# Optimization experiments

Measured on AMD Instinct MI355X. Metric: run time of the kernel, lower is better.

The kernel has to match this reference:

```python
import jax, jax.numpy as jnp
import numpy as np

B, C_IN, H, W = 8, 64, 256, 256
C_OUT, K, GROUPS, REP_DIM = 64, 3, 64, 512


def setup_inputs() -> dict:
    key = jax.random.key(0)
    k1, k2, k3 = jax.random.split(key, 3)
    x = jax.random.normal(k1, (B, C_IN, H, W), dtype=jnp.float32)
    representation = jax.random.normal(k2, (B, REP_DIM), dtype=jnp.float32)
    # Linear(representation_dim -> out_channels*k*k, bias=False) weight, [out_features, in_features]
    w_key = jax.random.normal(k3, (C_OUT * K * K, REP_DIM), dtype=jnp.float32) * (REP_DIM ** -0.5)
    return {"x": x, "representation": representation, "w_key": w_key}


def reference(x, representation, w_key):
    b = x.shape[0]
    fpg = C_IN // GROUPS          # features_per_group (input channels per group)
    opg = C_OUT // GROUPS         # output channels per group
    pad = K // 2

    # compress_key: Linear (no bias) + LeakyReLU(0.1)
    # per-sample dynamic kernels: [b, out_channels, k, k] (the repeat_interleave in the
    # original just copies this single spatial kernel across all fpg in-channels of a group)
    kern = jax.nn.leaky_relu(representation @ w_key.T, negative_slope=0.1)
    kern = kern.reshape(b, GROUPS, opg, K, K)

    # reflection pad (matches torch ReflectionPad2d)
    xp = jnp.pad(x, ((0, 0), (0, 0), (pad, pad), (pad, pad)), mode='reflect')

    # since each output channel's kernel is identical across its group's in-channels,
    # conv(sum of group channels) == sum of convs: pre-sum in-channels per group
    xg = xp.reshape(b, GROUPS, fpg, H + 2 * pad, W + 2 * pad).sum(axis=2)  # [b,g,hp,wp]

    # accumulate over the K*K kernel taps (small fixed loop), fully vectorized over b,g,h,w
    out = jnp.zeros((b, GROUPS, opg, H, W), dtype=x.dtype)
    for dy in range(K):
        for dx in range(K):
            out = out + jnp.einsum('bghw,bgo->bgohw',
                                   xg[:, :, dy:dy + H, dx:dx + W],
                                   kern[:, :, :, dy, dx])
    return out.reshape(b, C_OUT, H, W)
```

## Files before the change

kernel.cpp:

```cpp
#include <hip/hip_runtime.h>

typedef float f32x4 __attribute__((ext_vector_type(4)));

#define B_  8
#define C_  64
#define H_  256
#define W_  256
#define REP_ 512


#define RING 8
#define RPW  32

__global__ __launch_bounds__(256) void dwconv3x3_stream(const float* __restrict__ x,
                                                        const float* __restrict__ rep,
                                                        const float* __restrict__ wkey,
                                                        float* __restrict__ out) {
    int plane = blockIdx.x >> 1;
    int half  = blockIdx.x & 1;
    int wv   = threadIdx.x >> 6;
    int lane = threadIdx.x & 63;
    int b = plane >> 6;
    int c = plane & 63;

    __shared__ float kk[9];
    const float* rrow = rep + (size_t)b * REP_;
    for (int i = wv; i < 9; i += 4) {
        const float* wrow = wkey + (size_t)(c * 9 + i) * REP_;
        float acc = 0.f;
#pragma unroll
        for (int t = 0; t < REP_ / 64; ++t)
            acc += rrow[lane + t * 64] * wrow[lane + t * 64];
#pragma unroll
        for (int off = 32; off > 0; off >>= 1)
            acc += __shfl_xor(acc, off, 64);
        if (lane == 0)
            kk[i] = acc > 0.f ? acc : 0.1f * acc;
    }
    __syncthreads();

    float k[9];
#pragma unroll
    for (int i = 0; i < 9; ++i) k[i] = kk[i];

    int r0 = half * 128 + wv * RPW;
    int c4 = lane << 2;

    const float* pin  = x   + (size_t)plane * (H_ * W_);
    float*       pout = out + (size_t)plane * (H_ * W_);

    f32x4 raw[RING];
    float lft[RING], rgt[RING];

    auto issue = [&](int i) {
        int t = r0 - 1 + i;
        int rr = (t < 0) ? -t : ((t >= H_) ? (2 * H_ - 2 - t) : t);
        raw[i & 7] = *(const f32x4*)(pin + (size_t)rr * W_ + c4);
    };
    auto prep = [&](int i) {
        int s = i & 7;
        float lv = __shfl(raw[s][3], lane - 1, 64);
        lft[s] = (lane == 0) ? raw[s][1] : lv;
        float rv = __shfl(raw[s][0], lane + 1, 64);
        rgt[s] = (lane == 63) ? raw[s][2] : rv;
    };
    auto e = [&](int i, int t) -> float {
        int s = i & 7;
        if (t == 0) return lft[s];
        if (t == 5) return rgt[s];
        return raw[s][t - 1];
    };

#pragma unroll
    for (int i = 0; i < 5; ++i) issue(i);
    prep(0);
    prep(1);

#pragma unroll 1
    for (int it = 0; it < RPW / 8; ++it) {
#pragma unroll
        for (int u = 0; u < 8; ++u) {
            int j = it * 8 + u;
            issue(j + 5);
            prep(j + 2);
            f32x4 o4;
#pragma unroll
            for (int t = 0; t < 4; ++t) {
                o4[t] = k[0] * e(j, t)     + k[1] * e(j, t + 1)     + k[2] * e(j, t + 2)
                      + k[3] * e(j + 1, t) + k[4] * e(j + 1, t + 1) + k[5] * e(j + 1, t + 2)
                      + k[6] * e(j + 2, t) + k[7] * e(j + 2, t + 1) + k[8] * e(j + 2, t + 2);
            }
            __builtin_nontemporal_store(o4, (f32x4*)(pout + (size_t)(r0 + j) * W_ + c4));
        }
    }
}

extern "C" void kernel_launch(void* const* d_in, const int* in_sizes, int n_in,
                              void* d_out, int out_size, void* d_ws, size_t ws_size,
                              hipStream_t stream) {
    const float* x    = (const float*)d_in[0];
    const float* rep  = (const float*)d_in[1];
    const float* wkey = (const float*)d_in[2];
    float* out  = (float*)d_out;
    (void)d_ws; (void)ws_size;

    dwconv3x3_stream<<<1024, 256, 0, stream>>>(x, rep, wkey, out);
}
```

Before: 240.1 us.

## Stage input row bands into LDS via async global_load_lds before stencil

Replaces the per-wave register ring streaming with a band-per-block scheme: each block asynchronously loads 34 padded rows into LDS with global_load_lds, overlapping that with the kernel-weight dot products, then computes 32 output rows from LDS. The grid grows to 4096 blocks to raise parallelism and memory-level concurrency. This costs some halo re-read (34/32 rows), a full vmcnt wait before compute, and ~35KB of LDS per block, which limits occupancy. The per-block kernel-weight GEMV is now recomputed 8 times per plane instead of 2.

```diff
diff --git a/kernel.cpp b/kernel.cpp
--- a/kernel.cpp
+++ b/kernel.cpp
@@ -8,22 +8,38 @@
 #define W_  256
 #define REP_ 512
 
+#define BAND 32
+#define ROWS (BAND + 2)
 
-#define RING 8
-#define RPW  32
+__global__ __launch_bounds__(256) void dwconv3x3_lds(const float* __restrict__ x,
+                                                     const float* __restrict__ rep,
+                                                     const float* __restrict__ wkey,
+                                                     float* __restrict__ out) {
+    __shared__ float rows[ROWS][W_];
+    __shared__ float kk[9];
 
-__global__ __launch_bounds__(256) void dwconv3x3_stream(const float* __restrict__ x,
-                                                        const float* __restrict__ rep,
-                                                        const float* __restrict__ wkey,
-                                                        float* __restrict__ out) {
-    int plane = blockIdx.x >> 1;
-    int half  = blockIdx.x & 1;
+    int plane = blockIdx.x >> 3;
+    int band  = blockIdx.x & 7;
     int wv   = threadIdx.x >> 6;
     int lane = threadIdx.x & 63;
     int b = plane >> 6;
     int c = plane & 63;
 
-    __shared__ float kk[9];
+    const float* pin = x + (size_t)plane * (H_ * W_);
+
+    {
+        int t0 = band * BAND - 1;
+        for (int i = wv; i < ROWS; i += 4) {
+            int t = t0 + i;
+            int rr = (t < 0) ? -t : ((t >= H_) ? (2 * H_ - 2 - t) : t);
+            const float* src = pin + (size_t)rr * W_ + lane * 4;
+            __builtin_amdgcn_global_load_lds(
+                (const __attribute__((address_space(1))) void*)src,
+                (__attribute__((address_space(3))) void*)&rows[i][0],
+                16, 0, 0);
+        }
+    }
+
     const float* rrow = rep + (size_t)b * REP_;
     for (int i = wv; i < 9; i += 4) {
         const float* wrow = wkey + (size_t)(c * 9 + i) * REP_;
@@ -37,61 +53,44 @@
         if (lane == 0)
             kk[i] = acc > 0.f ? acc : 0.1f * acc;
     }
+
+    asm volatile("s_waitcnt vmcnt(0)" ::: "memory");
     __syncthreads();
 
     float k[9];
 #pragma unroll
     for (int i = 0; i < 9; ++i) k[i] = kk[i];
 
-    int r0 = half * 128 + wv * RPW;
+    float* pout = out + (size_t)plane * (H_ * W_);
     int c4 = lane << 2;
-
-    const float* pin  = x   + (size_t)plane * (H_ * W_);
-    float*       pout = out + (size_t)plane * (H_ * W_);
-
-    f32x4 raw[RING];
-    float lft[RING], rgt[RING];
-
-    auto issue = [&](int i) {
-        int t = r0 - 1 + i;
-        int rr = (t < 0) ? -t : ((t >= H_) ? (2 * H_ - 2 - t) : t);
-        raw[i & 7] = *(const f32x4*)(pin + (size_t)rr * W_ + c4);
-    };
-    auto prep = [&](int i) {
-        int s = i & 7;
-        float lv = __shfl(raw[s][3], lane - 1, 64);
-        lft[s] = (lane == 0) ? raw[s][1] : lv;
-        float rv = __shfl(raw[s][0], lane + 1, 64);
-        rgt[s] = (lane == 63) ? raw[s][2] : rv;
-    };
-    auto e = [&](int i, int t) -> float {
-        int s = i & 7;
-        if (t == 0) return lft[s];
-        if (t == 5) return rgt[s];
-        return raw[s][t - 1];
-    };
+    int jb = band * BAND + wv * 8;
 
 #pragma unroll
-    for (int i = 0; i < 5; ++i) issue(i);
-    prep(0);
-    prep(1);
+    for (int u = 0; u < 8; ++u) {
+        int li = wv * 8 + u;
+        f32x4 m0 = *(const f32x4*)&rows[li][c4];
+        f32x4 m1 = *(const f32x4*)&rows[li + 1][c4];
+        f32x4 m2 = *(const f32x4*)&rows[li + 2][c4];
+        float l0 = __shfl(m0[3], lane - 1, 64); l0 = (lane == 0) ? m0[1] : l0;
+        float l1 = __shfl(m1[3], lane - 1, 64); l1 = (lane == 0) ? m1[1] : l1;
+        float l2 = __shfl(m2[3], lane - 1, 64); l2 = (lane == 0) ? m2[1] : l2;
+        float r0 = __shfl(m0[0], lane + 1, 64); r0 = (lane == 63) ? m0[2] : r0;
+        float r1 = __shfl(m1[0], lane + 1, 64); r1 = (lane == 63) ? m1[2] : r1;
+        float r2 = __shfl(m2[0], lane + 1, 64); r2 = (lane == 63) ? m2[2] : r2;
 
-#pragma unroll 1
-    for (int it = 0; it < RPW / 8; ++it) {
+        auto E = [](const f32x4& m, float l, float r, int t) -> float {
+            if (t == 0) return l;
+            if (t == 5) return r;
+            return m[t - 1];
+        };
+        f32x4 o4;
 #pragma unroll
-        for (int u = 0; u < 8; ++u) {
-            int j = it * 8 + u;
-            issue(j + 5);
-            prep(j + 2);
-            f32x4 o4;
-#pragma unroll
-            for (int t = 0; t < 4; ++t) {
-                o4[t] = k[0] * e(j, t)     + k[1] * e(j, t + 1)     + k[2] * e(j, t + 2)
-                      + k[3] * e(j + 1, t) + k[4] * e(j + 1, t + 1) + k[5] * e(j + 1, t + 2)
-                      + k[6] * e(j + 2, t) + k[7] * e(j + 2, t + 1) + k[8] * e(j + 2, t + 2);
-            }
-            __builtin_nontemporal_store(o4, (f32x4*)(pout + (size_t)(r0 + j) * W_ + c4));
+        for (int t = 0; t < 4; ++t) {
+            o4[t] = k[0] * E(m0, l0, r0, t)     + k[1] * E(m0, l0, r0, t + 1) + k[2] * E(m0, l0, r0, t + 2)
+                  + k[3] * E(m1, l1, r1, t)     + k[4] * E(m1, l1, r1, t + 1) + k[5] * E(m1, l1, r1, t + 2)
+                  + k[6] * E(m2, l2, r2, t)     + k[7] * E(m2, l2, r2, t + 1) + k[8] * E(m2, l2, r2, t + 2);
         }
+        __builtin_nontemporal_store(o4, (f32x4*)(pout + (size_t)(jb + u) * W_ + c4));
     }
 }
 
@@ -104,5 +103,5 @@
     float* out  = (float*)d_out;
     (void)d_ws; (void)ws_size;
 
-    dwconv3x3_stream<<<1024, 256, 0, stream>>>(x, rep, wkey, out);
+    dwconv3x3_lds<<<4096, 256, 0, stream>>>(x, rep, wkey, out);
 }
```

Result: faster. 235.3 us (-2.0%).
